# Kernel tuning notes

Measured on AMD Instinct MI355X. Metric: run time of the kernel, lower is better.

The kernel has to match this reference:

```python
import jax, jax.numpy as jnp
import numpy as np

B, G, C, H, ZD, K, P = 2048, 2000, 50, 256, 32, 10, 4


def _xavier(key, shape, fan_in, fan_out):
    std = (2.0 / (fan_in + fan_out)) ** 0.5
    return std * jax.random.normal(key, shape, dtype=jnp.float32)


def setup_inputs() -> dict:
    key = jax.random.key(0)
    ks = jax.random.split(key, 13)
    X = jax.random.normal(ks[0], (B, G), dtype=jnp.float32)
    M = (jax.random.uniform(ks[1], (C, G)) < 0.1).astype(jnp.float32)
    # backbone: Linear(G,H) + LeakyReLU + Linear(H,H) + LeakyReLU (n_layer_enc=2)
    W1 = _xavier(ks[2], (G, H), G, H)
    b1 = jnp.zeros((H,), dtype=jnp.float32)
    W2 = _xavier(ks[3], (H, H), H, H)
    b2 = jnp.zeros((H,), dtype=jnp.float32)
    # MultiChannelLinear: w [C, ZD, H], b [1, C, ZD] (kaiming-uniform-ish init)
    bound_w = (6.0 / H) ** 0.5
    cw = jax.random.uniform(ks[4], (C, ZD, H), minval=-bound_w, maxval=bound_w, dtype=jnp.float32)
    bound_b = 1.0 / (H ** 0.5)
    cb = jax.random.uniform(ks[5], (1, C, ZD), minval=-bound_b, maxval=bound_b, dtype=jnp.float32)
    prototypes = _xavier(ks[6], (C, K, P, ZD), P * ZD, K)
    logvar = _xavier(ks[7], (C, K, P), P, K)
    c_bias = jnp.zeros((C, K), dtype=jnp.float32)
    bias = jnp.zeros((K,), dtype=jnp.float32)
    importance = _xavier(ks[8], (1, C), C, 1)
    return {"X": X, "M": M, "W1": W1, "b1": b1, "W2": W2, "b2": b2,
            "cw": cw, "cb": cb, "prototypes": prototypes, "logvar": logvar,
            "c_bias": c_bias, "bias": bias, "importance": importance}


def reference(X, M, W1, b1, W2, b2, cw, cb, prototypes, logvar, c_bias, bias, importance):
    # encode: mask input per concept, run shared MLP backbone, per-concept heads
    xm = X[:, None, :] * M[None]                       # [B, C, G]
    h = jax.nn.leaky_relu(jnp.einsum('bcg,gh->bch', xm, W1) + b1)
    h = jax.nn.leaky_relu(jnp.einsum('bch,hk->bck', h, W2) + b2)
    Z = jnp.einsum('bch,coh->bco', h, cw) + cb          # [B, C, ZD]
    # importance scores (dropout p=0 -> identity)
    imp = jnp.abs(importance)                           # [1, C]
    # broadcast squared distance to prototypes: [B, C, K, P]
    diff = Z[:, :, None, None, :] - prototypes[None]
    c2p_dist_sq = jnp.sum(diff * diff, axis=-1)
    scaled = c2p_dist_sq / (2.0 * jnp.exp(logvar))[None]
    c_logits = -jnp.min(scaled, axis=-1) + c_bias[None]  # [B, C, K]
    logits = jnp.log(jnp.sum(jnp.exp(c_logits) * imp[0][None, :, None] + 1e-16, axis=1)) + bias[None]
    return logits, c_logits
```

## Files before the change

kernel.cpp:

```cpp
#include <hip/hip_runtime.h>
#include <hip/hip_bf16.h>

#define NB   2048
#define NG   2000
#define NC   50
#define NH   256
#define NZD  32
#define NK   10
#define NP   4
#define BT   64
#define GS   2048
#define KP   320
#define NCH  10

typedef short short8  __attribute__((ext_vector_type(8)));
typedef short short4v __attribute__((ext_vector_type(4)));
typedef float f32x4   __attribute__((ext_vector_type(4)));
typedef unsigned int uint2v __attribute__((ext_vector_type(2)));

__device__ __forceinline__ unsigned short f2bf(float f) {
    union { float f; unsigned u; } v; v.f = f;
    unsigned r = v.u + 0x7fffu + ((v.u >> 16) & 1u);
    return (unsigned short)(r >> 16);
}

__device__ __forceinline__ unsigned cvt_pk_bf16(float lo, float hi) {
    unsigned r;
    asm("v_cvt_pk_bf16_f32 %0, %1, %2" : "=v"(r) : "v"(lo), "v"(hi));
    return r;
}

__device__ __forceinline__ void gld16(const unsigned short* g, char* l) {
    __builtin_amdgcn_global_load_lds(
        (const __attribute__((address_space(1))) unsigned int*)g,
        (__attribute__((address_space(3))) unsigned int*)l, 16, 0, 0);
}

__global__ void build_gidx(const float* __restrict__ M, int* __restrict__ gidx,
                           int* __restrict__ gcnt) {
    int c = blockIdx.x;
    int t = threadIdx.x;
    __shared__ int wcnt[4];
    __shared__ int base;
    if (t == 0) base = 0;
    __syncthreads();
    for (int g0 = 0; g0 < NG; g0 += 256) {
        int g = g0 + t;
        bool a = (g < NG) && (M[c * NG + g] != 0.0f);
        unsigned long long mask = __ballot(a);
        int lane = t & 63;
        int w = t >> 6;
        if (lane == 0) wcnt[w] = __popcll(mask);
        int pre = __popcll(mask & ((1ull << lane) - 1ull));
        __syncthreads();
        int woff = base;
        for (int i = 0; i < w; ++i) woff += wcnt[i];
        if (a) gidx[c * GS + woff + pre] = g;
        int tot = wcnt[0] + wcnt[1] + wcnt[2] + wcnt[3];
        __syncthreads();
        if (t == 0) base += tot;
        __syncthreads();
    }
    if (t == 0) gcnt[c] = base;
}

__global__ void prep_all(const float* __restrict__ X, const float* __restrict__ W1,
                         const float* __restrict__ W2, const float* __restrict__ cw,
                         const int* __restrict__ gidx, const int* __restrict__ gcnt,
                         unsigned short* __restrict__ xt, unsigned short* __restrict__ w1s,
                         unsigned short* __restrict__ w2s, unsigned short* __restrict__ cwb) {
    __shared__ float tile[64][65];
    const int bx = blockIdx.x;
    const int t  = threadIdx.x;
    if (bx < 1024) {
        int gb = bx & 31, bb = bx >> 5;
        int tx = t & 63, tq = t >> 6;
        #pragma unroll
        for (int i = 0; i < 16; ++i) {
            int r = tq * 16 + i;
            int gene = gb * 64 + tx;
            tile[r][tx] = (gene < NG) ? X[(size_t)(bb * 64 + r) * NG + gene] : 0.f;
        }
        __syncthreads();
        #pragma unroll
        for (int i = 0; i < 16; ++i) {
            int gl = tq * 16 + i;
            int gene = gb * 64 + gl;
            if (gene < NG)
                xt[(size_t)gene * NB + bb * 64 + tx] = f2bf(tile[tx][gl]);
        }
    } else if (bx < 1524) {
        int idx = bx - 1024;
        int ch = idx % NCH, c = idx / NCH;
        int col = t;
        int cnt = gcnt[c]; if (cnt > KP) cnt = KP;
        unsigned short v[32];
        #pragma unroll
        for (int kin = 0; kin < 32; ++kin) {
            int k = ch * 32 + kin;
            float x = 0.f;
            if (k < cnt) {
                int g = gidx[c * GS + k];
                x = W1[(size_t)g * NH + col];
            }
            v[kin] = f2bf(x);
        }
        unsigned short* dst = w1s + (((size_t)(c * NCH + ch)) * 256 + col) * 32;
        #pragma unroll
        for (int q = 0; q < 4; ++q) {
            short8 v8;
            #pragma unroll
            for (int i = 0; i < 8; ++i) v8[i] = (short)v[q * 8 + i];
            *(short8*)(dst + (q ^ ((col >> 1) & 3)) * 8) = v8;
        }
    } else if (bx < 1532) {
        int ch = bx - 1524;
        int col = t;
        unsigned short v[32];
        #pragma unroll
        for (int kin = 0; kin < 32; ++kin)
            v[kin] = f2bf(W2[(size_t)(ch * 32 + kin) * NH + col]);
        unsigned short* dst = w2s + ((size_t)ch * 256 + col) * 32;
        #pragma unroll
        for (int q = 0; q < 4; ++q) {
            short8 v8;
            #pragma unroll
            for (int i = 0; i < 8; ++i) v8[i] = (short)v[q * 8 + i];
            *(short8*)(dst + (q ^ ((col >> 1) & 3)) * 8) = v8;
        }
    } else {
        int c = bx - 1532;
        int o = t >> 3, seg = t & 7;
        #pragma unroll
        for (int blk = 0; blk < 4; ++blk) {
            int u = seg * 4 + blk;
            short8 v8;
            #pragma unroll
            for (int i = 0; i < 8; ++i)
                v8[i] = (short)f2bf(cw[((size_t)c * NZD + o) * NH + u * 8 + i]);
            *(short8*)(cwb + (size_t)c * 8192 + o * 256 + (u ^ (o & 7)) * 8) = v8;
        }
    }
}

#define PP_OFF   32768
#define WB0      40960
#define WB1      57344
#define LDS_BYTES 73728

__global__ __launch_bounds__(512, 4) void fused_mfma8(
    const unsigned short* __restrict__ xt,
    const unsigned short* __restrict__ w1s,
    const unsigned short* __restrict__ w2s,
    const unsigned short* __restrict__ cwb,
    const float* __restrict__ b1, const float* __restrict__ b2,
    const float* __restrict__ cb, const float* __restrict__ protos,
    const float* __restrict__ logvar, const float* __restrict__ c_bias,
    const int* __restrict__ gidx, const int* __restrict__ gcnt,
    float* __restrict__ out_cl)
{
    extern __shared__ char sm[];
    const int t  = threadIdx.x;
    const int l  = t & 63;
    const int w  = t >> 6;
    const int lr = l & 15;
    const int lg = l >> 4;
    const int wb = w >> 2;
    const int wh = w & 3;
    const int row0 = blockIdx.x * BT;
    const int c    = blockIdx.y;
    int cnt = gcnt[c]; if (cnt > KP) cnt = KP;
    const int nch = (cnt + 31) >> 5;

    auto Hb = [&](int r, int k) -> char* {
        return sm + r * 512 + ((((k >> 3) ^ (r & 7)) << 4) | ((k & 7) << 1));
    };
    auto XLb = [&](int r, int k) -> char* {
        return sm + r * 640 + ((((k >> 3) ^ (r & 7)) << 4) | ((k & 7) << 1));
    };
    auto stage_w = [&](const unsigned short* gsrc, int base) {
        gld16(gsrc + t * 8,        sm + base + t * 16);
        gld16(gsrc + 4096 + t * 8, sm + base + 8192 + t * 16);
    };
    auto aread = [&](int base, int col, int unit) -> short8 {
        return *(const short8*)(sm + base + col * 64 + ((unit ^ ((col >> 1) & 3)) << 4));
    };

    stage_w(w1s + (size_t)c * NCH * 8192, WB0);

    {
        const int gl2 = t & 63;
        const int rg  = t >> 6;
        short8 xv[5];
        int kk[5];
        #pragma unroll
        for (int i = 0; i < 5; ++i) {
            kk[i] = i * 64 + gl2;
            xv[i] = short8{0,0,0,0,0,0,0,0};
            if (kk[i] < cnt) {
                int g = gidx[c * GS + kk[i]];
                xv[i] = *(const short8*)(xt + (size_t)g * NB + row0 + rg * 8);
            }
        }
        #pragma unroll
        for (int i = 0; i < 5; ++i)
            #pragma unroll
            for (int j = 0; j < 8; ++j)
                *(short*)XLb(rg * 8 + j, kk[i]) = xv[i][j];
    }
    __syncthreads();

    f32x4 acc[2][4];
    #pragma unroll
    for (int nn = 0; nn < 2; ++nn)
        #pragma unroll
        for (int mm = 0; mm < 4; ++mm) acc[nn][mm] = f32x4{0.f, 0.f, 0.f, 0.f};

    for (int ch = 0; ch < nch; ++ch) {
        const int cur = (ch & 1) ? WB1 : WB0;
        const int nxt = (ch & 1) ? WB0 : WB1;
        if (ch + 1 < nch) stage_w(w1s + (size_t)(c * NCH + ch + 1) * 8192, nxt);
        else              stage_w(w2s, nxt);
        short8 a[4], b[2];
        #pragma unroll
        for (int mm = 0; mm < 4; ++mm)
            a[mm] = aread(cur, wh * 64 + mm * 16 + lr, lg);
        #pragma unroll
        for (int nn = 0; nn < 2; ++nn)
            b[nn] = *(const short8*)XLb(wb * 32 + nn * 16 + lr, ch * 32 + lg * 8);
        #pragma unroll
        for (int nn = 0; nn < 2; ++nn)
            #pragma unroll
            for (int mm = 0; mm < 4; ++mm)
                acc[nn][mm] = __builtin_amdgcn_mfma_f32_16x16x32_bf16(a[mm], b[nn], acc[nn][mm], 0, 0, 0);
        __syncthreads();
    }

    #pragma unroll
    for (int mm = 0; mm < 4; ++mm) {
        int k0 = wh * 64 + mm * 16 + lg * 4;
        f32x4 b1v = *(const f32x4*)(b1 + k0);
        #pragma unroll
        for (int nn = 0; nn < 2; ++nn) {
            int r = wb * 32 + nn * 16 + lr;
            float v0 = acc[nn][mm][0] + b1v[0]; v0 = (v0 >= 0.f) ? v0 : 0.01f * v0;
            float v1 = acc[nn][mm][1] + b1v[1]; v1 = (v1 >= 0.f) ? v1 : 0.01f * v1;
            float v2 = acc[nn][mm][2] + b1v[2]; v2 = (v2 >= 0.f) ? v2 : 0.01f * v2;
            float v3 = acc[nn][mm][3] + b1v[3]; v3 = (v3 >= 0.f) ? v3 : 0.01f * v3;
            uint2v pk;
            pk[0] = cvt_pk_bf16(v0, v1);
            pk[1] = cvt_pk_bf16(v2, v3);
            *(uint2v*)Hb(r, k0) = pk;
        }
    }
    __syncthreads();

    f32x4 acc2[2][4];
    #pragma unroll
    for (int nn = 0; nn < 2; ++nn)
        #pragma unroll
        for (int mm = 0; mm < 4; ++mm) acc2[nn][mm] = f32x4{0.f, 0.f, 0.f, 0.f};
    for (int ch2 = 0; ch2 < 8; ++ch2) {
        const int cur = ((nch + ch2) & 1) ? WB1 : WB0;
        const int nxt = ((nch + ch2) & 1) ? WB0 : WB1;
        if (ch2 + 1 < 8) stage_w(w2s + (size_t)(ch2 + 1) * 8192, nxt);
        else             stage_w(cwb + (size_t)c * 8192, nxt);
        short8 a[4], b[2];
        #pragma unroll
        for (int mm = 0; mm < 4; ++mm)
            a[mm] = aread(cur, wh * 64 + mm * 16 + lr, lg);
        #pragma unroll
        for (int nn = 0; nn < 2; ++nn)
            b[nn] = *(const short8*)Hb(wb * 32 + nn * 16 + lr, ch2 * 32 + lg * 8);
        #pragma unroll
        for (int nn = 0; nn < 2; ++nn)
            #pragma unroll
            for (int mm = 0; mm < 4; ++mm)
                acc2[nn][mm] = __builtin_amdgcn_mfma_f32_16x16x32_bf16(a[mm], b[nn], acc2[nn][mm], 0, 0, 0);
        __syncthreads();
    }
    const int cwbase = ((nch + 8) & 1) ? WB1 : WB0;
    const int szbase = ((nch + 8) & 1) ? WB0 : WB1;

    {
        #pragma unroll
        for (int mm = 0; mm < 4; ++mm) {
            int k0 = wh * 64 + mm * 16 + lg * 4;
            f32x4 b2v = *(const f32x4*)(b2 + k0);
            #pragma unroll
            for (int nn = 0; nn < 2; ++nn) {
                int r = wb * 32 + nn * 16 + lr;
                float v0 = acc2[nn][mm][0] + b2v[0]; v0 = (v0 >= 0.f) ? v0 : 0.01f * v0;
                float v1 = acc2[nn][mm][1] + b2v[1]; v1 = (v1 >= 0.f) ? v1 : 0.01f * v1;
                float v2 = acc2[nn][mm][2] + b2v[2]; v2 = (v2 >= 0.f) ? v2 : 0.01f * v2;
                float v3 = acc2[nn][mm][3] + b2v[3]; v3 = (v3 >= 0.f) ? v3 : 0.01f * v3;
                uint2v pk;
                pk[0] = cvt_pk_bf16(v0, v1);
                pk[1] = cvt_pk_bf16(v2, v3);
                *(uint2v*)Hb(r, k0) = pk;
            }
        }
        float* pp = (float*)(sm + PP_OFF);
        for (int i = t; i < NK * NP * NZD; i += 512)
            pp[(i >> 5) * 36 + (i & 31)] = protos[(size_t)c * (NK * NP * NZD) + i];
        if (t < NK * NP) pp[1440 + t] = 0.5f * expf(-logvar[c * (NK * NP) + t]);
        if (t < NK)      pp[1480 + t] = c_bias[c * NK + t];
    }
    __syncthreads();

    {
        const int rt = w & 3, ot = w >> 2;
        const int o = ot * 16 + lr;
        f32x4 az = f32x4{0.f, 0.f, 0.f, 0.f};
        #pragma unroll
        for (int ch = 0; ch < 8; ++ch) {
            short8 afr = *(const short8*)(sm + cwbase + o * 512 +
                                          ((((ch << 2) + lg) ^ (o & 7)) << 4));
            short8 bfr = *(const short8*)Hb(rt * 16 + lr, ch * 32 + lg * 8);
            az = __builtin_amdgcn_mfma_f32_16x16x32_bf16(afr, bfr, az, 0, 0, 0);
        }
        f32x4 cb4 = *(const f32x4*)(cb + c * NZD + ot * 16 + lg * 4);
        float* SZ = (float*)(sm + szbase);
        #pragma unroll
        for (int i = 0; i < 4; ++i)
            SZ[(rt * 16 + lr) * 36 + ot * 16 + lg * 4 + i] = az[i] + cb4[i];
    }
    __syncthreads();

    {
        const float* SZ  = (const float*)(sm + szbase);
        const float* pp  = (const float*)(sm + PP_OFF);
        const float* i2e = pp + 1440;
        const float* cbs = pp + 1480;
        const int rloc = (w & 3) * 16 + lr;
        f32x4 z[8];
        #pragma unroll
        for (int j = 0; j < 8; ++j)
            z[j] = *(const f32x4*)(SZ + rloc * 36 + j * 4);
        const int kk0 = (w >> 2) * 5;
        #pragma unroll
        for (int kk = kk0; kk < kk0 + 5; ++kk) {
            int kp = kk * NP + lg;
            f32x4 d = f32x4{0.f, 0.f, 0.f, 0.f};
            #pragma unroll
            for (int j = 0; j < 8; ++j) {
                f32x4 p = *(const f32x4*)(pp + kp * 36 + j * 4);
                f32x4 df = z[j] - p;
                d += df * df;
            }
            float sc = ((d[0] + d[1]) + (d[2] + d[3])) * i2e[kp];
            sc = fminf(sc, __shfl_xor(sc, 16));
            sc = fminf(sc, __shfl_xor(sc, 32));
            if (lg == 0)
                out_cl[((size_t)(row0 + rloc) * NC + c) * NK + kk] = cbs[kk] - sc;
        }
    }
}

__global__ __launch_bounds__(256, 1) void fused_main(
    const float* __restrict__ X,  const float* __restrict__ W1,
    const float* __restrict__ b1, const float* __restrict__ W2,
    const float* __restrict__ b2, const float* __restrict__ cw,
    const float* __restrict__ cb, const float* __restrict__ protos,
    const float* __restrict__ logvar, const float* __restrict__ c_bias,
    const int* __restrict__ gidx, const int* __restrict__ gcnt,
    float* __restrict__ out_cl)
{
    extern __shared__ float smemf[];
    float (*sh_big)[258] = (float (*)[258])smemf;
    float (*sh_w)[258]   = (float (*)[258])(smemf + 16512);
    float (*sh_x)[33]    = (float (*)[33])(smemf + 16512 + 8256);
    int*  sh_gid         = (int*)(smemf + 16512 + 8256 + 2112);

    const int t   = threadIdx.x;
    const int tx  = t & 15;
    const int ty  = t >> 4;
    const int row0 = blockIdx.x * BT;
    const int c    = blockIdx.y;

    float acc[4][16];
    #pragma unroll
    for (int i = 0; i < 4; ++i)
        #pragma unroll
        for (int l = 0; l < 16; ++l) acc[i][l] = 0.f;

    const int cnt = gcnt[c];
    const int nch = (cnt + 31) >> 5;
    for (int ch = 0; ch < nch; ++ch) {
        __syncthreads();
        if (t < 32) {
            int gi = ch * 32 + t;
            sh_gid[t] = (gi < cnt) ? gidx[c * GS + gi] : -1;
        }
        __syncthreads();
        #pragma unroll 4
        for (int jj = 0; jj < 32; ++jj) {
            int g = sh_gid[jj];
            sh_w[jj][t] = (g >= 0) ? W1[g * NH + t] : 0.f;
        }
        {
            int j  = t & 31;
            int rb2 = (t >> 5) * 8;
            int g  = sh_gid[j];
            #pragma unroll
            for (int ii = 0; ii < 8; ++ii)
                sh_x[rb2 + ii][j] = (g >= 0) ? X[(size_t)(row0 + rb2 + ii) * NG + g] : 0.f;
        }
        __syncthreads();
        #pragma unroll 8
        for (int j = 0; j < 32; ++j) {
            float xv[4];
            #pragma unroll
            for (int i = 0; i < 4; ++i) xv[i] = sh_x[ty * 4 + i][j];
            #pragma unroll
            for (int l = 0; l < 16; ++l) {
                float wv = sh_w[j][l * 16 + tx];
                #pragma unroll
                for (int i = 0; i < 4; ++i) acc[i][l] = fmaf(xv[i], wv, acc[i][l]);
            }
        }
    }
    #pragma unroll
    for (int i = 0; i < 4; ++i)
        #pragma unroll
        for (int l = 0; l < 16; ++l) {
            int col = l * 16 + tx;
            float v = acc[i][l] + b1[col];
            sh_big[ty * 4 + i][col] = (v >= 0.f) ? v : 0.01f * v;
        }

    float acc2[4][16];
    #pragma unroll
    for (int i = 0; i < 4; ++i)
        #pragma unroll
        for (int l = 0; l < 16; ++l) acc2[i][l] = 0.f;
    for (int ch = 0; ch < NH / 32; ++ch) {
        __syncthreads();
        #pragma unroll 4
        for (int jj = 0; jj < 32; ++jj)
            sh_w[jj][t] = W2[(size_t)(ch * 32 + jj) * NH + t];
        __syncthreads();
        #pragma unroll 8
        for (int j = 0; j < 32; ++j) {
            float xv[4];
            #pragma unroll
            for (int i = 0; i < 4; ++i) xv[i] = sh_big[ty * 4 + i][ch * 32 + j];
            #pragma unroll
            for (int l = 0; l < 16; ++l) {
                float wv = sh_w[j][l * 16 + tx];
                #pragma unroll
                for (int i = 0; i < 4; ++i) acc2[i][l] = fmaf(xv[i], wv, acc2[i][l]);
            }
        }
    }
    __syncthreads();
    #pragma unroll
    for (int i = 0; i < 4; ++i)
        #pragma unroll
        for (int l = 0; l < 16; ++l) {
            int col = l * 16 + tx;
            float v = acc2[i][l] + b2[col];
            sh_big[ty * 4 + i][col] = (v >= 0.f) ? v : 0.01f * v;
        }
    #pragma unroll 4
    for (int o = 0; o < NZD; ++o)
        sh_w[o][t] = cw[((size_t)c * NZD + o) * NH + t];
    __syncthreads();
    {
        int o  = t & 31;
        int rg = t >> 5;
        float cbv = cb[c * NZD + o];
        float zv[8];
        #pragma unroll
        for (int i = 0; i < 8; ++i) zv[i] = cbv;
        for (int h = 0; h < NH; ++h) {
            float wv = sh_w[o][h];
            #pragma unroll
            for (int i = 0; i < 8; ++i)
                zv[i] = fmaf(sh_big[rg * 8 + i][h], wv, zv[i]);
        }
        #pragma unroll
        for (int i = 0; i < 8; ++i) sh_x[rg * 8 + i][o] = zv[i];
    }
    __syncthreads();
    float* proto_s = &sh_w[0][0];
    float* i2e_s   = proto_s + NK * NP * NZD;
    float* cbias_s = i2e_s + NK * NP;
    for (int i = t; i < NK * NP * NZD; i += 256)
        proto_s[i] = protos[(size_t)c * NK * NP * NZD + i];
    if (t < NK * NP) i2e_s[t] = 0.5f * expf(-logvar[c * NK * NP + t]);
    if (t < NK)      cbias_s[t] = c_bias[c * NK + t];
    __syncthreads();
    for (int task = t; task < BT * NK; task += 256) {
        int r = task / NK;
        int k = task - r * NK;
        float best = 3.4e38f;
        #pragma unroll
        for (int p = 0; p < NP; ++p) {
            float d2 = 0.f;
            const float* ppr = proto_s + (k * NP + p) * NZD;
            #pragma unroll
            for (int o = 0; o < NZD; ++o) {
                float dv = sh_x[r][o] - ppr[o];
                d2 = fmaf(dv, dv, d2);
            }
            float sc = d2 * i2e_s[k * NP + p];
            best = fminf(best, sc);
        }
        out_cl[((size_t)(row0 + r) * NC + c) * NK + k] = cbias_s[k] - best;
    }
}

__global__ void reduce_logits(const float* __restrict__ cl,
                              const float* __restrict__ importance,
                              const float* __restrict__ bias,
                              float* __restrict__ out) {
    int idx = blockIdx.x * blockDim.x + threadIdx.x;
    if (idx >= NB * NK) return;
    int b = idx / NK;
    int k = idx - b * NK;
    float s = 0.f;
    for (int c = 0; c < NC; ++c) {
        float imp = fabsf(importance[c]);
        s += expf(cl[((size_t)b * NC + c) * NK + k]) * imp + 1e-16f;
    }
    out[idx] = logf(s) + bias[k];
}

extern "C" void kernel_launch(void* const* d_in, const int* in_sizes, int n_in,
                              void* d_out, int out_size, void* d_ws, size_t ws_size,
                              hipStream_t stream) {
    const float* X      = (const float*)d_in[0];
    const float* M      = (const float*)d_in[1];
    const float* W1     = (const float*)d_in[2];
    const float* b1     = (const float*)d_in[3];
    const float* W2     = (const float*)d_in[4];
    const float* b2     = (const float*)d_in[5];
    const float* cw     = (const float*)d_in[6];
    const float* cb     = (const float*)d_in[7];
    const float* protos = (const float*)d_in[8];
    const float* logvar = (const float*)d_in[9];
    const float* c_bias = (const float*)d_in[10];
    const float* bias   = (const float*)d_in[11];
    const float* imp    = (const float*)d_in[12];

    float* out_logits = (float*)d_out;
    float* out_cl     = out_logits + NB * NK;

    const size_t o_gcnt = (size_t)NC * GS * 4;
    const size_t o_w1s  = o_gcnt + 256;
    const size_t o_w2s  = o_w1s + (size_t)NC * NCH * 256 * 32 * 2;
    const size_t o_cwb  = o_w2s + (size_t)8 * 256 * 32 * 2;
    const size_t o_xt   = o_cwb + (size_t)NC * 32 * 256 * 2;
    const size_t need   = o_xt + (size_t)NG * NB * 2;

    int* gidx = (int*)d_ws;
    int* gcnt = (int*)((char*)d_ws + o_gcnt);
    unsigned short* w1s = (unsigned short*)((char*)d_ws + o_w1s);
    unsigned short* w2s = (unsigned short*)((char*)d_ws + o_w2s);
    unsigned short* cwb = (unsigned short*)((char*)d_ws + o_cwb);
    unsigned short* xt  = (unsigned short*)((char*)d_ws + o_xt);

    build_gidx<<<NC, 256, 0, stream>>>(M, gidx, gcnt);

    if (ws_size >= need) {
        prep_all<<<1582, 256, 0, stream>>>(X, W1, W2, cw, gidx, gcnt, xt, w1s, w2s, cwb);
        fused_mfma8<<<dim3(NB / BT, NC), 512, LDS_BYTES, stream>>>(
            xt, w1s, w2s, cwb, b1, b2, cb, protos, logvar, c_bias, gidx, gcnt, out_cl);
    } else {
        size_t smem = (size_t)(16512 + 8256 + 2112) * 4 + 32 * 4;
        fused_main<<<dim3(NB / BT, NC), 256, smem, stream>>>(
            X, W1, b1, W2, b2, cw, cb, protos, logvar, c_bias, gidx, gcnt, out_cl);
    }
    reduce_logits<<<(NB * NK + 255) / 256, 256, 0, stream>>>(out_cl, imp, bias, out_logits);
}
```

Baseline: 90.75 us.

## Read W2 and head weights directly from global instead of LDS staging

The layer-2 and per-concept head GEMMs now load their A fragments straight from global memory (L2-resident bf16 weights) rather than double-buffering them through LDS. This removes eight per-chunk barriers and the associated async LDS copies, and the layer-2 loop is fully unrolled. The index-building kernel also switches to 1024-thread blocks with 16 wave counters. The trade-off is higher global and L2 load latency on every MFMA fragment, with no LDS reuse across waves.

Measured after the change: 87.30 us. 1.04x faster.

```diff
diff --git a/kernel.cpp b/kernel.cpp
--- a/kernel.cpp
+++ b/kernel.cpp
@@ -40,11 +40,11 @@
                            int* __restrict__ gcnt) {
     int c = blockIdx.x;
     int t = threadIdx.x;
-    __shared__ int wcnt[4];
+    __shared__ int wcnt[16];
     __shared__ int base;
     if (t == 0) base = 0;
     __syncthreads();
-    for (int g0 = 0; g0 < NG; g0 += 256) {
+    for (int g0 = 0; g0 < NG; g0 += 1024) {
         int g = g0 + t;
         bool a = (g < NG) && (M[c * NG + g] != 0.0f);
         unsigned long long mask = __ballot(a);
@@ -56,7 +56,9 @@
         int woff = base;
         for (int i = 0; i < w; ++i) woff += wcnt[i];
         if (a) gidx[c * GS + woff + pre] = g;
-        int tot = wcnt[0] + wcnt[1] + wcnt[2] + wcnt[3];
+        int tot = 0;
+        #pragma unroll
+        for (int i = 0; i < 16; ++i) tot += wcnt[i];
         __syncthreads();
         if (t == 0) base += tot;
         __syncthreads();
@@ -148,7 +150,7 @@
 #define WB1      57344
 #define LDS_BYTES 73728
 
-__global__ __launch_bounds__(512, 4) void fused_mfma8(
+__global__ __launch_bounds__(512, 4) void fused_mfma10(
     const unsigned short* __restrict__ xt,
     const unsigned short* __restrict__ w1s,
     const unsigned short* __restrict__ w2s,
@@ -178,15 +180,16 @@
     auto XLb = [&](int r, int k) -> char* {
         return sm + r * 640 + ((((k >> 3) ^ (r & 7)) << 4) | ((k & 7) << 1));
     };
-    auto stage_w = [&](const unsigned short* gsrc, int base) {
-        gld16(gsrc + t * 8,        sm + base + t * 16);
-        gld16(gsrc + 4096 + t * 8, sm + base + 8192 + t * 16);
+    auto stage_w1 = [&](int ch, int base) {
+        const unsigned short* g = w1s + ((size_t)(c * NCH + ch)) * 8192;
+        gld16(g + t * 8,        sm + base + t * 16);
+        gld16(g + 4096 + t * 8, sm + base + 8192 + t * 16);
     };
     auto aread = [&](int base, int col, int unit) -> short8 {
         return *(const short8*)(sm + base + col * 64 + ((unit ^ ((col >> 1) & 3)) << 4));
     };
 
-    stage_w(w1s + (size_t)c * NCH * 8192, WB0);
+    stage_w1(0, WB0);
 
     {
         const int gl2 = t & 63;
@@ -219,8 +222,7 @@
     for (int ch = 0; ch < nch; ++ch) {
         const int cur = (ch & 1) ? WB1 : WB0;
         const int nxt = (ch & 1) ? WB0 : WB1;
-        if (ch + 1 < nch) stage_w(w1s + (size_t)(c * NCH + ch + 1) * 8192, nxt);
-        else              stage_w(w2s, nxt);
+        if (ch + 1 < nch) stage_w1(ch + 1, nxt);
         short8 a[4], b[2];
         #pragma unroll
         for (int mm = 0; mm < 4; ++mm)
@@ -260,15 +262,15 @@
     for (int nn = 0; nn < 2; ++nn)
         #pragma unroll
         for (int mm = 0; mm < 4; ++mm) acc2[nn][mm] = f32x4{0.f, 0.f, 0.f, 0.f};
+    #pragma unroll
     for (int ch2 = 0; ch2 < 8; ++ch2) {
-        const int cur = ((nch + ch2) & 1) ? WB1 : WB0;
-        const int nxt = ((nch + ch2) & 1) ? WB0 : WB1;
-        if (ch2 + 1 < 8) stage_w(w2s + (size_t)(ch2 + 1) * 8192, nxt);
-        else             stage_w(cwb + (size_t)c * 8192, nxt);
         short8 a[4], b[2];
         #pragma unroll
-        for (int mm = 0; mm < 4; ++mm)
-            a[mm] = aread(cur, wh * 64 + mm * 16 + lr, lg);
+        for (int mm = 0; mm < 4; ++mm) {
+            int col = wh * 64 + mm * 16 + lr;
+            a[mm] = *(const short8*)(w2s + ((size_t)ch2 * 256 + col) * 32 +
+                                     ((lg ^ ((col >> 1) & 3)) << 3));
+        }
         #pragma unroll
         for (int nn = 0; nn < 2; ++nn)
             b[nn] = *(const short8*)Hb(wb * 32 + nn * 16 + lr, ch2 * 32 + lg * 8);
@@ -277,10 +279,8 @@
             #pragma unroll
             for (int mm = 0; mm < 4; ++mm)
                 acc2[nn][mm] = __builtin_amdgcn_mfma_f32_16x16x32_bf16(a[mm], b[nn], acc2[nn][mm], 0, 0, 0);
-        __syncthreads();
-    }
-    const int cwbase = ((nch + 8) & 1) ? WB1 : WB0;
-    const int szbase = ((nch + 8) & 1) ? WB0 : WB1;
+    }
+    __syncthreads();
 
     {
         #pragma unroll
@@ -314,13 +314,13 @@
         f32x4 az = f32x4{0.f, 0.f, 0.f, 0.f};
         #pragma unroll
         for (int ch = 0; ch < 8; ++ch) {
-            short8 afr = *(const short8*)(sm + cwbase + o * 512 +
-                                          ((((ch << 2) + lg) ^ (o & 7)) << 4));
+            short8 afr = *(const short8*)(cwb + (size_t)c * 8192 + o * 256 +
+                                          ((((ch << 2) + lg) ^ (o & 7)) << 3));
             short8 bfr = *(const short8*)Hb(rt * 16 + lr, ch * 32 + lg * 8);
             az = __builtin_amdgcn_mfma_f32_16x16x32_bf16(afr, bfr, az, 0, 0, 0);
         }
         f32x4 cb4 = *(const f32x4*)(cb + c * NZD + ot * 16 + lg * 4);
-        float* SZ = (float*)(sm + szbase);
+        float* SZ = (float*)(sm + WB0);
         #pragma unroll
         for (int i = 0; i < 4; ++i)
             SZ[(rt * 16 + lr) * 36 + ot * 16 + lg * 4 + i] = az[i] + cb4[i];
@@ -328,7 +328,7 @@
     __syncthreads();
 
     {
-        const float* SZ  = (const float*)(sm + szbase);
+        const float* SZ  = (const float*)(sm + WB0);
         const float* pp  = (const float*)(sm + PP_OFF);
         const float* i2e = pp + 1440;
         const float* cbs = pp + 1480;
@@ -375,7 +375,7 @@
     const int t   = threadIdx.x;
     const int tx  = t & 15;
     const int ty  = t >> 4;
-    const int row0 = blockIdx.x * BT;
+    const int row0 = blockIdx.x * 64;
     const int c    = blockIdx.y;
 
     float acc[4][16];
@@ -491,7 +491,7 @@
     if (t < NK * NP) i2e_s[t] = 0.5f * expf(-logvar[c * NK * NP + t]);
     if (t < NK)      cbias_s[t] = c_bias[c * NK + t];
     __syncthreads();
-    for (int task = t; task < BT * NK; task += 256) {
+    for (int task = t; task < 64 * NK; task += 256) {
         int r = task / NK;
         int k = task - r * NK;
         float best = 3.4e38f;
@@ -520,6 +520,7 @@
     int b = idx / NK;
     int k = idx - b * NK;
     float s = 0.f;
+    #pragma unroll
     for (int c = 0; c < NC; ++c) {
         float imp = fabsf(importance[c]);
         s += expf(cl[((size_t)b * NC + c) * NK + k]) * imp + 1e-16f;
@@ -561,15 +562,15 @@
     unsigned short* cwb = (unsigned short*)((char*)d_ws + o_cwb);
     unsigned short* xt  = (unsigned short*)((char*)d_ws + o_xt);
 
-    build_gidx<<<NC, 256, 0, stream>>>(M, gidx, gcnt);
+    build_gidx<<<NC, 1024, 0, stream>>>(M, gidx, gcnt);
 
     if (ws_size >= need) {
         prep_all<<<1582, 256, 0, stream>>>(X, W1, W2, cw, gidx, gcnt, xt, w1s, w2s, cwb);
-        fused_mfma8<<<dim3(NB / BT, NC), 512, LDS_BYTES, stream>>>(
+        fused_mfma10<<<dim3(NB / BT, NC), 512, LDS_BYTES, stream>>>(
             xt, w1s, w2s, cwb, b1, b2, cb, protos, logvar, c_bias, gidx, gcnt, out_cl);
     } else {
         size_t smem = (size_t)(16512 + 8256 + 2112) * 4 + 32 * 4;
-        fused_main<<<dim3(NB / BT, NC), 256, smem, stream>>>(
+        fused_main<<<dim3(NB / 64, NC), 256, smem, stream>>>(
             X, W1, b1, W2, b2, cw, cb, protos, logvar, c_bias, gidx, gcnt, out_cl);
     }
     reduce_logits<<<(NB * NK + 255) / 256, 256, 0, stream>>>(out_cl, imp, bias, out_logits);
```
